# Performance work log

Hardware: AMD Instinct MI355X
Metric: run time of the kernel (lower is better)

Reference implementation:

```python
import jax, jax.numpy as jnp
import numpy as np

B, D, O, K = 8192, 256, 256, 16


def setup_inputs() -> dict:
    key = jax.random.key(0)
    k1, k2, k3, k4 = jax.random.split(key, 4)
    x = jax.random.normal(k1, (B, D), dtype=jnp.float32)
    # learned params
    values = jax.random.uniform(k2, (O, D, K), dtype=jnp.float32, minval=-0.05, maxval=0.05)
    skip_w = jax.random.normal(k3, (O, D), dtype=jnp.float32) * (1.0 / np.sqrt(D))
    skip_b = jax.random.uniform(k4, (O,), dtype=jnp.float32, minval=-1.0, maxval=1.0) / np.sqrt(D)
    # fixed buffer (non-trainable)
    grid = jnp.linspace(-1.0, 1.0, K).astype(jnp.float32)
    return {"x": x, "values": values, "skip_w": skip_w, "skip_b": skip_b, "grid": grid}


def reference(x, values, skip_w, skip_b, grid):
    # x: [B, D]; values: [O, D, K]; grid: [K]
    num_knots = grid.shape[0]
    xc = jnp.clip(x, -1.0, 1.0)
    # torch.bucketize(x, grid) (right=False) == searchsorted side='left'
    right = jnp.searchsorted(grid, xc, side="left")            # [B, D]
    left = jnp.clip(right - 1, 0, num_knots - 2)               # [B, D]
    right = left + 1
    g0 = grid[left]
    g1 = grid[right]
    w = (xc - g0) / (g1 - g0 + 1e-12)                          # [B, D]
    # sparse linear-interp coefficients over knots: 2 nonzeros per (b, d)
    coeff = (1.0 - w)[..., None] * jax.nn.one_hot(left, num_knots, dtype=xc.dtype) \
          + w[..., None] * jax.nn.one_hot(right, num_knots, dtype=xc.dtype)  # [B, D, K]
    # y[b,o] = sum_d sum_k coeff[b,d,k] * values[o,d,k]  (== per-dim gather+interp+accumulate)
    y = jnp.einsum("bdk,odk->bo", coeff, values)
    y = y + xc @ skip_w.T + skip_b
    return y
```

## Files before the change

kernel.cpp:

```cpp
#include <hip/hip_runtime.h>
#include <hip/hip_bf16.h>
#include <stdint.h>


#define D_DIM  256
#define O_DIM  256
#define BM     128
#define NTHR   256

typedef __attribute__((ext_vector_type(8))) short bf16x8;
typedef __attribute__((ext_vector_type(4))) float f32x4;

__global__ __launch_bounds__(256) void kan_prep(
    const float* __restrict__ values,
    const float* __restrict__ skip_w,
    const float* __restrict__ gknots,
    unsigned short* __restrict__ Vp)
{
    int tid = blockIdx.x * blockDim.x + threadIdx.x;
    int e = tid * 8;
    int o = e >> 12;
    int kflat = e & 4095;
    float sw = skip_w[(o << 8) | (kflat >> 4)];
    int kmod = kflat & 15;

    const float4* vp4 = reinterpret_cast<const float4*>(values + e);
    float4 v0 = vp4[0], v1 = vp4[1];
    float f[8] = {v0.x, v0.y, v0.z, v0.w, v1.x, v1.y, v1.z, v1.w};
    unsigned int w[4];
#pragma unroll
    for (int j = 0; j < 4; ++j) {
        float2 ab;
        ab.x = f[2*j]     + gknots[kmod + 2*j]     * sw;
        ab.y = f[2*j + 1] + gknots[kmod + 2*j + 1] * sw;
        __hip_bfloat162 p2 = __float22bfloat162_rn(ab);
        __builtin_memcpy(&w[j], &p2, 4);
    }
    size_t c = (size_t)(kflat >> 3) * 256 + (size_t)o;
    *reinterpret_cast<uint4*>(Vp + c * 8) = make_uint4(w[0], w[1], w[2], w[3]);
}

template<int KS>
__global__ __launch_bounds__(NTHR, 2) void kan_gemm(
    const float* __restrict__ x,
    const unsigned short* __restrict__ Vp,
    float* __restrict__ part)
{
    __shared__ unsigned long long Pk[128 * 64];

    constexpr int ITERS = 64 / KS;
    const int t    = threadIdx.x;
    const int lane = t & 63;
    const int wid  = t >> 6;
    const int wm   = wid >> 1;
    const int wn   = wid & 1;
    const int l15  = lane & 15;
    const int lhi  = lane >> 4;

    const int bid = (int)blockIdx.x;
    const int ks  = bid & (KS - 1);
    const int nt  = (bid >> 2) & 1;
    const int mt  = bid >> 3;
    const int bm0 = mt * BM;
    const int nc0 = nt * 128;
    const size_t kc0 = (size_t)ks * (512 / KS);

    char* pb = (char*)&Pk[0];

    {
        int row = t >> 1;
        int half = (t & 1) * 32;
        const float* xr = x + (size_t)(bm0 + row) * D_DIM + ks * (256 / KS) + half;
        int rs = (row & 7) << 2;
#pragma unroll
        for (int j4 = 0; j4 < 8; ++j4) {
            float4 xv = reinterpret_cast<const float4*>(xr)[j4];
            float v[4] = {xv.x, xv.y, xv.z, xv.w};
#pragma unroll
            for (int e = 0; e < 4; ++e) {
                int dloc = half + j4 * 4 + e;
                float xc = fminf(1.f, fmaxf(-1.f, v[e]));
                float tt = (xc + 1.f) * 7.5f;
                int li = (int)tt;
                li = li > 14 ? 14 : li;
                float w1 = tt - (float)li;
                float2 cw; cw.x = 1.f - w1; cw.y = w1;
                __hip_bfloat162 p2 = __float22bfloat162_rn(cw);
                unsigned int pkw;
                __builtin_memcpy(&pkw, &p2, 4);
                unsigned long long q8 =
                    ((unsigned long long)pkw << ((li & 1) << 4)) |
                    ((unsigned long long)(unsigned)(li >> 1) << 48);
                int kt = dloc >> 2, p = (dloc >> 1) & 1, g = dloc & 1;
                int s = kt * 2 + g;
                *reinterpret_cast<unsigned long long*>(
                    pb + row * 512 + ((s ^ rs) << 4) + p * 8) = q8;
            }
        }
    }
    __syncthreads();

    const unsigned jbase = (unsigned)((lhi & 1) * 4);
    const int g = lhi >> 1;
    int prow[4], prs[4];
#pragma unroll
    for (int mi = 0; mi < 4; ++mi) {
        int row = wm * 64 + mi * 16 + l15;
        prow[mi] = row * 512;
        prs[mi] = (row & 7) << 2;
    }

    #define LOADB(BG, KT)                                                      \
        {                                                                      \
            const unsigned short* _b = Vp + (kc0 + (size_t)(KT) * 8) * 2048;   \
            _Pragma("unroll")                                                  \
            for (int kh = 0; kh < 2; ++kh)                                     \
                _Pragma("unroll")                                              \
                for (int ni = 0; ni < 4; ++ni) {                               \
                    int n = nc0 + wn * 64 + ni * 16 + l15;                     \
                    BG[kh * 4 + ni] = *reinterpret_cast<const bf16x8*>(        \
                        _b + ((size_t)((kh * 4 + lhi) * 256 + n)) * 8);        \
                }                                                              \
        }

    auto mkfrag = [&](unsigned lo, unsigned hi) -> bf16x8 {
        unsigned jd = (hi >> 16) - jbase;
        unsigned hc = hi & 0xffffu;
        uint4 w;
        w.x = (jd == 0u) ? lo : ((jd + 1u == 0u) ? hc : 0u);
        w.y = (jd == 1u) ? lo : ((jd == 0u) ? hc : 0u);
        w.z = (jd == 2u) ? lo : ((jd == 1u) ? hc : 0u);
        w.w = (jd == 3u) ? lo : ((jd == 2u) ? hc : 0u);
        bf16x8 r;
        __builtin_memcpy(&r, &w, 16);
        return r;
    };

    f32x4 acc[4][4] = {};
    bf16x8 bgA[8], bgB[8];

    LOADB(bgA, 0);

    #define ITERBODY(KT, BGC, BGN)                                            \
        {                                                                     \
            const bool last = (KT) == ITERS - 1;                              \
            if (!last) LOADB(BGN, (KT) + 1);                                  \
            uint4 q[4];                                                       \
            _Pragma("unroll")                                                 \
            for (int mi = 0; mi < 4; ++mi)                                    \
                q[mi] = *reinterpret_cast<const uint4*>(                      \
                    pb + prow[mi] + ((((KT) * 2 + g) ^ prs[mi]) << 4));       \
            bf16x8 af[4];                                                     \
            _Pragma("unroll")                                                 \
            for (int mi = 0; mi < 4; ++mi)                                    \
                af[mi] = mkfrag(q[mi].x, q[mi].y);                            \
            __builtin_amdgcn_s_setprio(1);                                    \
            _Pragma("unroll")                                                 \
            for (int mi = 0; mi < 4; ++mi)                                    \
                _Pragma("unroll")                                             \
                for (int ni = 0; ni < 4; ++ni)                                \
                    acc[mi][ni] = __builtin_amdgcn_mfma_f32_16x16x32_bf16(    \
                        af[mi], BGC[ni], acc[mi][ni], 0, 0, 0);               \
            __builtin_amdgcn_s_setprio(0);                                    \
            _Pragma("unroll")                                                 \
            for (int mi = 0; mi < 4; ++mi)                                    \
                af[mi] = mkfrag(q[mi].z, q[mi].w);                            \
            __builtin_amdgcn_s_setprio(1);                                    \
            _Pragma("unroll")                                                 \
            for (int mi = 0; mi < 4; ++mi)                                    \
                _Pragma("unroll")                                             \
                for (int ni = 0; ni < 4; ++ni)                                \
                    acc[mi][ni] = __builtin_amdgcn_mfma_f32_16x16x32_bf16(    \
                        af[mi], BGC[4 + ni], acc[mi][ni], 0, 0, 0);           \
            __builtin_amdgcn_s_setprio(0);                                    \
        }

    for (int t2 = 0; t2 < ITERS / 2; ++t2) {
        ITERBODY(2 * t2,     bgA, bgB);
        ITERBODY(2 * t2 + 1, bgB, bgA);
    }
    #undef ITERBODY
    #undef LOADB

    float* dst = part + (size_t)ks * (8192 * 256);
#pragma unroll
    for (int ni = 0; ni < 4; ++ni) {
        int col = nc0 + wn * 64 + ni * 16 + l15;
#pragma unroll
        for (int mi = 0; mi < 4; ++mi) {
            f32x4 v = acc[mi][ni];
            int row0 = bm0 + wm * 64 + mi * 16 + lhi * 4;
#pragma unroll
            for (int r = 0; r < 4; ++r)
                dst[(size_t)(row0 + r) * O_DIM + col] = v[r];
        }
    }
}

__global__ __launch_bounds__(256) void kan_reduce(
    const float* __restrict__ part,
    const float* __restrict__ skip_b,
    float* __restrict__ out,
    int nparts)
{
    size_t i4 = (size_t)blockIdx.x * 256 + threadIdx.x;
    size_t e = i4 * 4;
    f32x4 s = *reinterpret_cast<const f32x4*>(&skip_b[e & 255]);
    for (int p = 0; p < nparts; ++p)
        s += *reinterpret_cast<const f32x4*>(part + (size_t)p * (8192 * 256) + e);
    *reinterpret_cast<f32x4*>(out + e) = s;
}

__global__ __launch_bounds__(256) void kan_naive(
    const float* __restrict__ x,
    const unsigned short* __restrict__ Vp,
    const float* __restrict__ skip_b,
    float* __restrict__ out)
{
    int b = blockIdx.x, o = threadIdx.x;
    float acc = skip_b[o];
    for (int d = 0; d < 256; ++d) {
        float xc = fminf(1.f, fmaxf(-1.f, x[(size_t)b * 256 + d]));
        float tt = (xc + 1.f) * 7.5f;
        int li = (int)tt; li = li > 14 ? 14 : li;
        float w1 = tt - (float)li;
        int k0 = d * 16 + li;
        unsigned short u0 = Vp[((size_t)(k0 >> 3) * 256 + o) * 8 + (k0 & 7)];
        int k1 = k0 + 1;
        unsigned short u1 = Vp[((size_t)(k1 >> 3) * 256 + o) * 8 + (k1 & 7)];
        float f0 = __uint_as_float((unsigned)u0 << 16);
        float f1 = __uint_as_float((unsigned)u1 << 16);
        acc += (1.f - w1) * f0 + w1 * f1;
    }
    out[(size_t)b * 256 + o] = acc;
}

extern "C" void kernel_launch(void* const* d_in, const int* in_sizes, int n_in,
                              void* d_out, int out_size, void* d_ws, size_t ws_size,
                              hipStream_t stream) {
    const float* x      = (const float*)d_in[0];
    const float* values = (const float*)d_in[1];
    const float* skip_w = (const float*)d_in[2];
    const float* skip_b = (const float*)d_in[3];
    const float* gknots = (const float*)d_in[4];
    float* out = (float*)d_out;
    (void)in_sizes; (void)n_in; (void)out_size;

    unsigned short* Vp = (unsigned short*)d_ws;
    float* part = (float*)((char*)d_ws + 2 * 1024 * 1024);

    kan_prep<<<dim3(512), dim3(256), 0, stream>>>(values, skip_w, gknots, Vp);

    const size_t need = 2u * 1024 * 1024 + (size_t)4 * 8192 * 256 * 4;
    if (ws_size >= need) {
        kan_gemm<4><<<dim3(512), dim3(NTHR), 0, stream>>>(x, Vp, part);
        kan_reduce<<<dim3(2048), dim3(256), 0, stream>>>(part, skip_b, out, 4);
    } else {
        kan_naive<<<dim3(8192), dim3(256), 0, stream>>>(x, Vp, skip_b, out);
    }
}
```

Before: 42.40 us.

## Halve split-K and fuse partial reduction into GEMM via atomic last-block counter

Split-K drops from 4 to 2, so the grid shrinks from 512 to 256 blocks with launch bounds of one block per SM. Each block now builds its packed coefficient tile in two halves to fit shared memory. The separate reduce kernel is replaced by an atomic per-tile counter: the second block to finish sums both partials plus the bias and writes the output. This removes a kernel launch and halves the partial-buffer traffic, at the cost of a memset launch, fewer blocks to hide latency, and an extra mid-loop barrier.

```diff
diff --git a/kernel.cpp b/kernel.cpp
--- a/kernel.cpp
+++ b/kernel.cpp
@@ -6,6 +6,7 @@
 #define D_DIM  256
 #define O_DIM  256
 #define BM     128
+#define ITERS  32
 #define NTHR   256
 
 typedef __attribute__((ext_vector_type(8))) short bf16x8;
@@ -40,15 +41,17 @@
     *reinterpret_cast<uint4*>(Vp + c * 8) = make_uint4(w[0], w[1], w[2], w[3]);
 }
 
-template<int KS>
-__global__ __launch_bounds__(NTHR, 2) void kan_gemm(
+__global__ __launch_bounds__(NTHR, 1) void kan_gemm(
     const float* __restrict__ x,
     const unsigned short* __restrict__ Vp,
-    float* __restrict__ part)
+    const float* __restrict__ skip_b,
+    float* __restrict__ part,
+    int* __restrict__ cnt,
+    float* __restrict__ out)
 {
     __shared__ unsigned long long Pk[128 * 64];
-
-    constexpr int ITERS = 64 / KS;
+    __shared__ int sflag;
+
     const int t    = threadIdx.x;
     const int lane = t & 63;
     const int wid  = t >> 6;
@@ -58,19 +61,19 @@
     const int lhi  = lane >> 4;
 
     const int bid = (int)blockIdx.x;
-    const int ks  = bid & (KS - 1);
-    const int nt  = (bid >> 2) & 1;
-    const int mt  = bid >> 3;
+    const int ks  = bid & 1;
+    const int nt  = (bid >> 1) & 1;
+    const int mt  = bid >> 2;
     const int bm0 = mt * BM;
     const int nc0 = nt * 128;
-    const size_t kc0 = (size_t)ks * (512 / KS);
+    const size_t kc0 = (size_t)ks * 256;
 
     char* pb = (char*)&Pk[0];
 
-    {
+    auto buildPk = [&](int w) {
         int row = t >> 1;
         int half = (t & 1) * 32;
-        const float* xr = x + (size_t)(bm0 + row) * D_DIM + ks * (256 / KS) + half;
+        const float* xr = x + (size_t)(bm0 + row) * D_DIM + ks * 128 + w * 64 + half;
         int rs = (row & 7) << 2;
 #pragma unroll
         for (int j4 = 0; j4 < 8; ++j4) {
@@ -91,14 +94,13 @@
                 unsigned long long q8 =
                     ((unsigned long long)pkw << ((li & 1) << 4)) |
                     ((unsigned long long)(unsigned)(li >> 1) << 48);
-                int kt = dloc >> 2, p = (dloc >> 1) & 1, g = dloc & 1;
-                int s = kt * 2 + g;
+                int kt = dloc >> 2, p = (dloc >> 1) & 1, g2 = dloc & 1;
+                int s = kt * 2 + g2;
                 *reinterpret_cast<unsigned long long*>(
                     pb + row * 512 + ((s ^ rs) << 4) + p * 8) = q8;
             }
         }
-    }
-    __syncthreads();
+    };
 
     const unsigned jbase = (unsigned)((lhi & 1) * 4);
     const int g = lhi >> 1;
@@ -139,6 +141,8 @@
     f32x4 acc[4][4] = {};
     bf16x8 bgA[8], bgB[8];
 
+    buildPk(0);
+    __syncthreads();
     LOADB(bgA, 0);
 
     #define ITERBODY(KT, BGC, BGN)                                            \
@@ -149,7 +153,7 @@
             _Pragma("unroll")                                                 \
             for (int mi = 0; mi < 4; ++mi)                                    \
                 q[mi] = *reinterpret_cast<const uint4*>(                      \
-                    pb + prow[mi] + ((((KT) * 2 + g) ^ prs[mi]) << 4));       \
+                    pb + prow[mi] + (((((KT) & 15) * 2 + g) ^ prs[mi]) << 4));\
             bf16x8 af[4];                                                     \
             _Pragma("unroll")                                                 \
             for (int mi = 0; mi < 4; ++mi)                                    \
@@ -176,6 +180,11 @@
         }
 
     for (int t2 = 0; t2 < ITERS / 2; ++t2) {
+        if (t2 == ITERS / 4) {
+            __syncthreads();
+            buildPk(1);
+            __syncthreads();
+        }
         ITERBODY(2 * t2,     bgA, bgB);
         ITERBODY(2 * t2 + 1, bgB, bgA);
     }
@@ -195,20 +204,26 @@
                 dst[(size_t)(row0 + r) * O_DIM + col] = v[r];
         }
     }
-}
-
-__global__ __launch_bounds__(256) void kan_reduce(
-    const float* __restrict__ part,
-    const float* __restrict__ skip_b,
-    float* __restrict__ out,
-    int nparts)
-{
-    size_t i4 = (size_t)blockIdx.x * 256 + threadIdx.x;
-    size_t e = i4 * 4;
-    f32x4 s = *reinterpret_cast<const f32x4*>(&skip_b[e & 255]);
-    for (int p = 0; p < nparts; ++p)
-        s += *reinterpret_cast<const f32x4*>(part + (size_t)p * (8192 * 256) + e);
-    *reinterpret_cast<f32x4*>(out + e) = s;
+
+    __threadfence();
+    if (t == 0) sflag = atomicAdd(&cnt[mt * 2 + nt], 1);
+    __syncthreads();
+    if (sflag == 1) {
+        __threadfence();
+        const float* p0 = part;
+        const float* p1 = part + (size_t)8192 * 256;
+#pragma unroll
+        for (int i = 0; i < 16; ++i) {
+            int c = t + 256 * i;
+            int row = bm0 + (c >> 5);
+            int col = nc0 + (c & 31) * 4;
+            size_t off = (size_t)row * O_DIM + col;
+            f32x4 a = *reinterpret_cast<const f32x4*>(p0 + off);
+            f32x4 b = *reinterpret_cast<const f32x4*>(p1 + off);
+            f32x4 sb = *reinterpret_cast<const f32x4*>(skip_b + col);
+            *reinterpret_cast<f32x4*>(out + off) = a + b + sb;
+        }
+    }
 }
 
 __global__ __launch_bounds__(256) void kan_naive(
@@ -247,14 +262,18 @@
     (void)in_sizes; (void)n_in; (void)out_size;
 
     unsigned short* Vp = (unsigned short*)d_ws;
-    float* part = (float*)((char*)d_ws + 2 * 1024 * 1024);
+    float* part = (float*)((char*)d_ws + 2u * 1024 * 1024);
+    int* cnt = (int*)((char*)d_ws + 2u * 1024 * 1024
+                      + (size_t)2 * 8192 * 256 * sizeof(float));
 
     kan_prep<<<dim3(512), dim3(256), 0, stream>>>(values, skip_w, gknots, Vp);
 
-    const size_t need = 2u * 1024 * 1024 + (size_t)4 * 8192 * 256 * 4;
+    const size_t need = 2u * 1024 * 1024
+                      + (size_t)2 * 8192 * 256 * sizeof(float) + 512;
     if (ws_size >= need) {
-        kan_gemm<4><<<dim3(512), dim3(NTHR), 0, stream>>>(x, Vp, part);
-        kan_reduce<<<dim3(2048), dim3(256), 0, stream>>>(part, skip_b, out, 4);
+        hipMemsetAsync(cnt, 0, 128 * sizeof(int), stream);
+        kan_gemm<<<dim3(256), dim3(NTHR), 0, stream>>>(
+            x, Vp, skip_b, part, cnt, out);
     } else {
         kan_naive<<<dim3(8192), dim3(256), 0, stream>>>(x, Vp, skip_b, out);
     }
```

After: 101.2 us. 2.39x slower.
